# Kernel optimization log

Hardware: AMD Instinct MI355X
Metric: run time of the kernel (lower is better)

## Reference

```python
import jax, jax.numpy as jnp
import numpy as np

# H36M parent-child joint pairs (the second assignment in the source overrides the first)
PARENT = np.array([[0,1],[1,2],[2,3],[0,4],[4,5],[5,6],[0,8],[8,14],[14,15],[15,16],[8,11],[11,12],[12,13],[8,10]])
NUM_JOINTS = 17
NUM_PAIRS = 14
GRID = 64


def create_heatmap(joint2d, size):
    # Gaussian with cov = 2*I evaluated on integer grid, normalized by its max.
    # Original: grid[i, j] = N([i, j]; mean=[x, y], 2I) / max -> pdf constant cancels.
    xy = joint2d * 64.0  # (B, J, 2)
    ii = jnp.arange(size, dtype=joint2d.dtype)
    dx = ii[None, None, :, None] - xy[..., 0][..., None, None]  # (B, J, size, 1)
    dy = ii[None, None, None, :] - xy[..., 1][..., None, None]  # (B, J, 1, size)
    d2 = dx * dx + dy * dy  # (B, J, size, size)
    g = jnp.exp(-d2 / 4.0)  # exp(-d2 / (2*var)), var = 2
    return g / jnp.max(g, axis=(2, 3), keepdims=True)


def setup_inputs() -> dict:
    key = jax.random.key(0)
    k1, k2, k3, k4 = jax.random.split(key, 4)
    B = 256
    return {
        "pred": jax.random.normal(k1, (B, NUM_JOINTS, 3), dtype=jnp.float32),
        "joints": jax.random.normal(k2, (B, NUM_JOINTS, 3), dtype=jnp.float32),
        "middle_out": jax.random.normal(k3, (B, NUM_JOINTS + 3 * NUM_PAIRS, GRID, GRID), dtype=jnp.float32),
        "joint2d": jax.random.uniform(k4, (B, NUM_JOINTS, 2), dtype=jnp.float32),
    }


def reference(pred, joints, middle_out, joint2d):
    eps = 0.1
    B, _, H, W = middle_out.shape
    # l3D: joints last dim == 3 branch
    l3d = jnp.mean(jnp.sum(jnp.abs(joints - pred[:, :NUM_JOINTS, :]), axis=(1, 2)))

    heatmap = create_heatmap(joint2d, H)  # (B, 17, 64, 64)

    # L2D: mean over batch of sum over joints of squared Frobenius norm (detached in original)
    diff = middle_out[:, :NUM_JOINTS] - heatmap
    L2D = jnp.mean(jnp.sum(jnp.sum(diff * diff, axis=(2, 3)), axis=1))

    # LHEM: vectorized heatmap triplets over batch and all 14 parent/child pairs
    p_idx = PARENT[:, 0]
    c_idx = PARENT[:, 1]
    hp = heatmap[:, p_idx]  # (B, 14, 64, 64)
    hc = heatmap[:, c_idx]  # (B, 14, 64, 64)
    d = joints[:, p_idx, 2] - joints[:, c_idx, 2]  # (B, 14)
    r = jnp.where(d > eps, 1, jnp.where(jnp.abs(d) < eps, 0, -1))[..., None, None]
    ch0 = jnp.where(r == -1, hc, 0.0)
    ch1 = jnp.where(r == 0, hp + hc, hp)
    ch2 = jnp.where(r == 1, hc, 0.0)
    T_GT = jnp.stack((ch0, ch1, ch2), axis=2)  # (B, 14, 3, 64, 64)
    T_pred = middle_out[:, NUM_JOINTS:NUM_JOINTS + 3 * NUM_PAIRS].reshape(B, NUM_PAIRS, 3, H, W)
    norms = jnp.sqrt(jnp.sum((T_GT - T_pred) ** 2, axis=(3, 4)))  # (B, 14, 3)
    LHEM = jnp.mean(jnp.sum(jnp.sum(norms, axis=2) ** 2, axis=1))

    Lint = 0.005 * (LHEM + L2D)
    # Original computes L2D / LHEM in detached numpy -> no gradient through Lint
    return l3d + jax.lax.stop_gradient(Lint)
```

## Files before the change

### kernel.cpp

```cpp
#include <hip/hip_runtime.h>
#include <math.h>

#define NJ 17
#define NP 14
#define NCH 59
#define BATCH 256
#define PSTRIDE 64

__constant__ int c_par0[NP] = {0, 1, 2, 0, 4, 5, 0, 8, 14, 15, 8, 11, 12, 8};
__constant__ int c_par1[NP] = {1, 2, 3, 4, 5, 6, 8, 14, 15, 16, 11, 12, 13, 10};

__device__ __forceinline__ float wave_reduce(float v) {
    #pragma unroll
    for (int off = 32; off; off >>= 1) v += __shfl_down(v, off, 64);
    return v;
}

__device__ __forceinline__ void heat_params(const float* __restrict__ joint2d,
                                            int b, int j,
                                            float& x, float& y, float& m) {
    x = joint2d[(b * NJ + j) * 2 + 0] * 64.f;
    y = joint2d[(b * NJ + j) * 2 + 1] * 64.f;
    const float rx = fminf(fmaxf(floorf(x + 0.5f), 0.f), 63.f);
    const float ry = fminf(fmaxf(floorf(y + 0.5f), 0.f), 63.f);
    m = (rx - x) * (rx - x) + (ry - y) * (ry - y);
}

__global__ __launch_bounds__(256) void slice_sum_kernel(
    const float* __restrict__ pred,
    const float* __restrict__ joints,
    const float* __restrict__ middle,
    const float* __restrict__ joint2d,
    float* __restrict__ partial)
{
    const int c    = blockIdx.x;
    const int lane = threadIdx.x & 63;
    const int b    = (blockIdx.y << 2) | (threadIdx.x >> 6);

    const float4* __restrict__ src =
        (const float4*)(middle + ((size_t)b * NCH + c) * 4096) + lane;
    float4 d[16];
    #pragma unroll
    for (int j = 0; j < 16; ++j) d[j] = src[64 * j];

    float wp = 0.f, wc = 0.f;
    int jp = 0, jc = 0;
    if (c < NJ) {
        jp = c; wp = 1.f;
    } else {
        const int pi = c - NJ;
        const int p  = pi / 3;
        const int ch = pi - p * 3;
        jp = c_par0[p];
        jc = c_par1[p];
        const float dz = joints[(b * NJ + jp) * 3 + 2] - joints[(b * NJ + jc) * 3 + 2];
        const int rs = (dz > 0.1f) ? 1 : ((fabsf(dz) < 0.1f) ? 0 : -1);
        if (ch == 0)      { wp = 0.f; wc = (rs == -1) ? 1.f : 0.f; }
        else if (ch == 1) { wp = 1.f; wc = (rs ==  0) ? 1.f : 0.f; }
        else              { wp = 0.f; wc = (rs ==  1) ? 1.f : 0.f; }
    }

    float xp = 0.f, yp = 0.f, mp = 0.f;
    float xq = 0.f, yq = 0.f, mq = 0.f;
    if (wp != 0.f) heat_params(joint2d, b, jp, xp, yp, mp);
    if (wc != 0.f) heat_params(joint2d, b, jc, xq, yq, mq);

    const float col0 = (float)((4 * lane) & 63);
    const float row0 = (float)(lane >> 4);
    float cEp[4] = {0.f, 0.f, 0.f, 0.f};
    float cEc[4] = {0.f, 0.f, 0.f, 0.f};
    if (wp != 0.f) {
        #pragma unroll
        for (int q = 0; q < 4; ++q) {
            const float dy = (col0 + (float)q) - yp;
            cEp[q] = __expf(-0.25f * dy * dy);
        }
    }
    if (wc != 0.f) {
        #pragma unroll
        for (int q = 0; q < 4; ++q) {
            const float dy = (col0 + (float)q) - yq;
            cEc[q] = __expf(-0.25f * dy * dy);
        }
    }
    const float mp4 = 0.25f * mp;
    const float mq4 = 0.25f * mq;

    float acc = 0.f;
    #pragma unroll
    for (int j = 0; j < 16; ++j) {
        const float fi = row0 + (float)(4 * j);
        float rEp = 0.f, rEc = 0.f;
        if (wp != 0.f) {
            const float dx = fi - xp;
            rEp = __expf(fmaf(-0.25f * dx, dx, mp4));
        }
        if (wc != 0.f) {
            const float dx = fi - xq;
            rEc = __expf(fmaf(-0.25f * dx, dx, mq4));
        }
        const float mv[4] = {d[j].x, d[j].y, d[j].z, d[j].w};
        #pragma unroll
        for (int q = 0; q < 4; ++q) {
            const float tgt = fmaf(rEc, cEc[q], rEp * cEp[q]);
            const float df = tgt - mv[q];
            acc = fmaf(df, df, acc);
        }
    }

    acc = wave_reduce(acc);
    if (lane == 0) partial[b * PSTRIDE + c] = acc;

    if (c == 0) {
        float v = 0.f;
        if (lane < NJ * 3) {
            const int i = b * NJ * 3 + lane;
            v = fabsf(joints[i] - pred[i]);
        }
        v = wave_reduce(v);
        if (lane == 0) partial[b * PSTRIDE + 59] = v;
    }
}

__global__ __launch_bounds__(256) void finalize_kernel(
    const float* __restrict__ partial,
    float* __restrict__ out)
{
    const int b = threadIdx.x;
    const float4* __restrict__ row = (const float4*)(partial + b * PSTRIDE);
    float4 r[15];
    #pragma unroll
    for (int i = 0; i < 15; ++i) r[i] = row[i];
    const float* pr = (const float*)r;

    float l2d = 0.f;
    #pragma unroll
    for (int c = 0; c < NJ; ++c) l2d += pr[c];

    float hem = 0.f;
    #pragma unroll
    for (int p = 0; p < NP; ++p) {
        const float n = sqrtf(pr[NJ + 3 * p + 0]) +
                        sqrtf(pr[NJ + 3 * p + 1]) +
                        sqrtf(pr[NJ + 3 * p + 2]);
        hem = fmaf(n, n, hem);
    }

    double v = ((double)pr[59] + 0.005 * ((double)l2d + (double)hem)) * (1.0 / BATCH);

    #pragma unroll
    for (int off = 32; off; off >>= 1) v += __shfl_down(v, off, 64);
    __shared__ double sh[4];
    if ((b & 63) == 0) sh[b >> 6] = v;
    __syncthreads();
    if (b == 0) out[0] = (float)(sh[0] + sh[1] + sh[2] + sh[3]);
}

extern "C" void kernel_launch(void* const* d_in, const int* in_sizes, int n_in,
                              void* d_out, int out_size, void* d_ws, size_t ws_size,
                              hipStream_t stream) {
    const float* pred    = (const float*)d_in[0];
    const float* joints  = (const float*)d_in[1];
    const float* middle  = (const float*)d_in[2];
    const float* joint2d = (const float*)d_in[3];
    float* out  = (float*)d_out;
    float* part = (float*)d_ws;

    dim3 grid(NCH, BATCH / 4);
    slice_sum_kernel<<<grid, 256, 0, stream>>>(pred, joints, middle, joint2d, part);
    finalize_kernel<<<1, 256, 0, stream>>>(part, out);
}
```

Before: 340.3 us.

## Use persistent waves with double-buffered register prefetch of slices

```diff
diff --git a/kernel.cpp b/kernel.cpp
--- a/kernel.cpp
+++ b/kernel.cpp
@@ -5,6 +5,8 @@
 #define NP 14
 #define NCH 59
 #define BATCH 256
+#define NS (BATCH * NCH)
+#define NWAVES 2048
 #define PSTRIDE 64
 
 __constant__ int c_par0[NP] = {0, 1, 2, 0, 4, 5, 0, 8, 14, 15, 8, 11, 12, 8};
@@ -26,100 +28,123 @@
     m = (rx - x) * (rx - x) + (ry - y) * (ry - y);
 }
 
-__global__ __launch_bounds__(256) void slice_sum_kernel(
+__global__ __launch_bounds__(256, 2) void slice_sum_kernel(
     const float* __restrict__ pred,
     const float* __restrict__ joints,
     const float* __restrict__ middle,
     const float* __restrict__ joint2d,
     float* __restrict__ partial)
 {
-    const int c    = blockIdx.x;
     const int lane = threadIdx.x & 63;
-    const int b    = (blockIdx.y << 2) | (threadIdx.x >> 6);
+    const int w    = (blockIdx.x << 2) | (threadIdx.x >> 6);
 
-    const float4* __restrict__ src =
-        (const float4*)(middle + ((size_t)b * NCH + c) * 4096) + lane;
-    float4 d[16];
-    #pragma unroll
-    for (int j = 0; j < 16; ++j) d[j] = src[64 * j];
+    float4 bufA[16], bufB[16];
 
-    float wp = 0.f, wc = 0.f;
-    int jp = 0, jc = 0;
-    if (c < NJ) {
-        jp = c; wp = 1.f;
-    } else {
-        const int pi = c - NJ;
-        const int p  = pi / 3;
-        const int ch = pi - p * 3;
-        jp = c_par0[p];
-        jc = c_par1[p];
-        const float dz = joints[(b * NJ + jp) * 3 + 2] - joints[(b * NJ + jc) * 3 + 2];
-        const int rs = (dz > 0.1f) ? 1 : ((fabsf(dz) < 0.1f) ? 0 : -1);
-        if (ch == 0)      { wp = 0.f; wc = (rs == -1) ? 1.f : 0.f; }
-        else if (ch == 1) { wp = 1.f; wc = (rs ==  0) ? 1.f : 0.f; }
-        else              { wp = 0.f; wc = (rs ==  1) ? 1.f : 0.f; }
+    #define ISSUE(sid, buf)                                                    \
+        {                                                                      \
+            const float4* __restrict__ src =                                   \
+                (const float4*)(middle + (size_t)(sid) * 4096) + lane;         \
+            _Pragma("unroll")                                                  \
+            for (int j = 0; j < 16; ++j) (buf)[j] = src[64 * j];               \
+        }
+
+    #define PROCESS(sid, buf)                                                  \
+        {                                                                      \
+            const int b = (sid) / NCH;                                         \
+            const int c = (sid) - b * NCH;                                     \
+            float wp = 0.f, wc = 0.f;                                          \
+            int jp = 0, jc = 0;                                                \
+            if (c < NJ) {                                                      \
+                jp = c; wp = 1.f;                                              \
+            } else {                                                           \
+                const int pi = c - NJ;                                         \
+                const int p  = pi / 3;                                         \
+                const int ch = pi - p * 3;                                     \
+                jp = c_par0[p];                                                \
+                jc = c_par1[p];                                                \
+                const float dz = joints[(b * NJ + jp) * 3 + 2] -               \
+                                 joints[(b * NJ + jc) * 3 + 2];                \
+                const int rs = (dz > 0.1f) ? 1 : ((fabsf(dz) < 0.1f) ? 0 : -1);\
+                if (ch == 0)      { wp = 0.f; wc = (rs == -1) ? 1.f : 0.f; }   \
+                else if (ch == 1) { wp = 1.f; wc = (rs ==  0) ? 1.f : 0.f; }   \
+                else              { wp = 0.f; wc = (rs ==  1) ? 1.f : 0.f; }   \
+            }                                                                  \
+            float xp = 0.f, yp = 0.f, mp = 0.f;                                \
+            float xq = 0.f, yq = 0.f, mq = 0.f;                                \
+            if (wp != 0.f) heat_params(joint2d, b, jp, xp, yp, mp);            \
+            if (wc != 0.f) heat_params(joint2d, b, jc, xq, yq, mq);            \
+            const float col0 = (float)((4 * lane) & 63);                       \
+            const float row0 = (float)(lane >> 4);                             \
+            float cEp[4] = {0.f, 0.f, 0.f, 0.f};                               \
+            float cEc[4] = {0.f, 0.f, 0.f, 0.f};                               \
+            if (wp != 0.f) {                                                   \
+                _Pragma("unroll")                                              \
+                for (int q = 0; q < 4; ++q) {                                  \
+                    const float dy = (col0 + (float)q) - yp;                   \
+                    cEp[q] = __expf(-0.25f * dy * dy);                         \
+                }                                                              \
+            }                                                                  \
+            if (wc != 0.f) {                                                   \
+                _Pragma("unroll")                                              \
+                for (int q = 0; q < 4; ++q) {                                  \
+                    const float dy = (col0 + (float)q) - yq;                   \
+                    cEc[q] = __expf(-0.25f * dy * dy);                         \
+                }                                                              \
+            }                                                                  \
+            const float mp4 = 0.25f * mp;                                      \
+            const float mq4 = 0.25f * mq;                                      \
+            float acc = 0.f;                                                   \
+            _Pragma("unroll")                                                  \
+            for (int j = 0; j < 16; ++j) {                                     \
+                const float fi = row0 + (float)(4 * j);                        \
+                float rEp = 0.f, rEc = 0.f;                                    \
+                if (wp != 0.f) {                                               \
+                    const float dx = fi - xp;                                  \
+                    rEp = __expf(fmaf(-0.25f * dx, dx, mp4));                  \
+                }                                                              \
+                if (wc != 0.f) {                                               \
+                    const float dx = fi - xq;                                  \
+                    rEc = __expf(fmaf(-0.25f * dx, dx, mq4));                  \
+                }                                                              \
+                const float mv[4] = {(buf)[j].x, (buf)[j].y,                   \
+                                     (buf)[j].z, (buf)[j].w};                  \
+                _Pragma("unroll")                                              \
+                for (int q = 0; q < 4; ++q) {                                  \
+                    const float tgt = fmaf(rEc, cEc[q], rEp * cEp[q]);         \
+                    const float df = tgt - mv[q];                              \
+                    acc = fmaf(df, df, acc);                                   \
+                }                                                              \
+            }                                                                  \
+            acc = wave_reduce(acc);                                            \
+            if (lane == 0) partial[b * PSTRIDE + c] = acc;                     \
+            if (c == 0) {                                                      \
+                float v = 0.f;                                                 \
+                if (lane < NJ * 3) {                                           \
+                    const int i = b * NJ * 3 + lane;                           \
+                    v = fabsf(joints[i] - pred[i]);                            \
+                }                                                              \
+                v = wave_reduce(v);                                            \
+                if (lane == 0) partial[b * PSTRIDE + 59] = v;                  \
+            }                                                                  \
+        }
+
+    int sid = w;
+    ISSUE(sid, bufA);
+    while (true) {
+        int nxt = sid + NWAVES;
+        if (nxt < NS) ISSUE(nxt, bufB);
+        PROCESS(sid, bufA);
+        sid = nxt;
+        if (sid >= NS) break;
+
+        nxt = sid + NWAVES;
+        if (nxt < NS) ISSUE(nxt, bufA);
+        PROCESS(sid, bufB);
+        sid = nxt;
+        if (sid >= NS) break;
     }
-
-    float xp = 0.f, yp = 0.f, mp = 0.f;
-    float xq = 0.f, yq = 0.f, mq = 0.f;
-    if (wp != 0.f) heat_params(joint2d, b, jp, xp, yp, mp);
-    if (wc != 0.f) heat_params(joint2d, b, jc, xq, yq, mq);
-
-    const float col0 = (float)((4 * lane) & 63);
-    const float row0 = (float)(lane >> 4);
-    float cEp[4] = {0.f, 0.f, 0.f, 0.f};
-    float cEc[4] = {0.f, 0.f, 0.f, 0.f};
-    if (wp != 0.f) {
-        #pragma unroll
-        for (int q = 0; q < 4; ++q) {
-            const float dy = (col0 + (float)q) - yp;
-            cEp[q] = __expf(-0.25f * dy * dy);
-        }
-    }
-    if (wc != 0.f) {
-        #pragma unroll
-        for (int q = 0; q < 4; ++q) {
-            const float dy = (col0 + (float)q) - yq;
-            cEc[q] = __expf(-0.25f * dy * dy);
-        }
-    }
-    const float mp4 = 0.25f * mp;
-    const float mq4 = 0.25f * mq;
-
-    float acc = 0.f;
-    #pragma unroll
-    for (int j = 0; j < 16; ++j) {
-        const float fi = row0 + (float)(4 * j);
-        float rEp = 0.f, rEc = 0.f;
-        if (wp != 0.f) {
-            const float dx = fi - xp;
-            rEp = __expf(fmaf(-0.25f * dx, dx, mp4));
-        }
-        if (wc != 0.f) {
-            const float dx = fi - xq;
-            rEc = __expf(fmaf(-0.25f * dx, dx, mq4));
-        }
-        const float mv[4] = {d[j].x, d[j].y, d[j].z, d[j].w};
-        #pragma unroll
-        for (int q = 0; q < 4; ++q) {
-            const float tgt = fmaf(rEc, cEc[q], rEp * cEp[q]);
-            const float df = tgt - mv[q];
-            acc = fmaf(df, df, acc);
-        }
-    }
-
-    acc = wave_reduce(acc);
-    if (lane == 0) partial[b * PSTRIDE + c] = acc;
-
-    if (c == 0) {
-        float v = 0.f;
-        if (lane < NJ * 3) {
-            const int i = b * NJ * 3 + lane;
-            v = fabsf(joints[i] - pred[i]);
-        }
-        v = wave_reduce(v);
-        if (lane == 0) partial[b * PSTRIDE + 59] = v;
-    }
+    #undef ISSUE
+    #undef PROCESS
 }
 
 __global__ __launch_bounds__(256) void finalize_kernel(
@@ -166,7 +191,7 @@
     float* out  = (float*)d_out;
     float* part = (float*)d_ws;
 
-    dim3 grid(NCH, BATCH / 4);
-    slice_sum_kernel<<<grid, 256, 0, stream>>>(pred, joints, middle, joint2d, part);
+    slice_sum_kernel<<<NWAVES / 4, 256, 0, stream>>>(pred, joints, middle,
+                                                     joint2d, part);
     finalize_kernel<<<1, 256, 0, stream>>>(part, out);
 }
```

Result: slower. 348.3 us (+2.3%).
